# Kernel tuning notes

Measured on AMD Instinct MI355X. Metric: run time of the kernel, lower is better.

The kernel has to match this reference:

```python
import jax, jax.numpy as jnp
import numpy as np

NBINS = 256

def _equalize_flat(flat):
    # flat: [N, P] int32 pixel values in [0,255], N = B*C channels, P = H*W pixels
    N, P = flat.shape
    hist = jax.vmap(lambda v: jnp.bincount(v, length=NBINS))(flat)  # [N, 256]
    bins = jnp.arange(NBINS, dtype=jnp.int32)
    # last nonzero bin value per channel (PIL: drop last nonzero entry from the step sum)
    last_idx = jnp.max(jnp.where(hist != 0, bins[None, :], -1), axis=1)  # [N]
    last_val = jnp.take_along_axis(hist, last_idx[:, None], axis=1)[:, 0]  # [N]
    step = (P - last_val) // 255  # [N] integer floor div
    safe_step = jnp.maximum(step, 1)
    cs = jnp.cumsum(hist, axis=1)  # [N, 256]
    lut = (cs + (step // 2)[:, None]) // safe_step[:, None]
    # pad left with 0, drop last, clamp to [0,255]
    lut = jnp.concatenate([jnp.zeros((N, 1), lut.dtype), lut[:, :-1]], axis=1)
    lut = jnp.clip(lut, 0, 255)
    eq = jnp.take_along_axis(lut, flat, axis=1)  # [N, P]
    # channels with step==0 pass through unchanged
    return jnp.where((step == 0)[:, None], flat, eq)


def setup_inputs() -> dict:
    key = jax.random.key(0)
    img = jax.random.randint(key, (64, 3, 512, 512), 0, 256).astype(jnp.float32)
    return {"img": img}


def reference(img) -> jnp.ndarray:
    B, C, H, W = img.shape
    flat = img.astype(jnp.int32).reshape(B * C, H * W)
    out = _equalize_flat(flat)
    return out.reshape(B, C, H, W).astype(img.dtype)
```

## Files before the change

### kernel.cpp

```cpp
#include <hip/hip_runtime.h>


#define NBINS 256
#define BPC 32

__global__ __launch_bounds__(256) void eq_hist_kernel(
    const float* __restrict__ in, unsigned int* __restrict__ ghist,
    int P, int bpc) {
    __shared__ unsigned int lh[NBINS * 32];
    const int t = threadIdx.x;
    const int copy = t & 31;

    for (int i = t; i < NBINS * 32; i += 256) lh[i] = 0u;
    __syncthreads();

    const int chan = blockIdx.x / bpc;
    const int blk  = blockIdx.x % bpc;
    const int chunk = P / bpc;
    const float4* base =
        (const float4*)(in + (size_t)chan * P + (size_t)blk * chunk);
    const int nvec = chunk / 4;

    for (int i = t; i < nvec; i += 256) {
        float4 v = base[i];
        int ix = min(max((int)v.x, 0), 255);
        int iy = min(max((int)v.y, 0), 255);
        int iz = min(max((int)v.z, 0), 255);
        int iw = min(max((int)v.w, 0), 255);
        atomicAdd(&lh[ix * 32 + copy], 1u);
        atomicAdd(&lh[iy * 32 + copy], 1u);
        atomicAdd(&lh[iz * 32 + copy], 1u);
        atomicAdd(&lh[iw * 32 + copy], 1u);
    }
    __syncthreads();

    unsigned int s = 0;
    #pragma unroll
    for (int c = 0; c < 32; ++c)
        s += lh[t * 32 + ((t + c) & 31)];
    atomicAdd(&ghist[chan * NBINS + t], s);
}

__global__ __launch_bounds__(256) void eq_lut_kernel(
    const unsigned int* __restrict__ ghist, float* __restrict__ glut, int P) {
    __shared__ unsigned int s[NBINS];
    __shared__ int sidx[NBINS];
    const int t = threadIdx.x;
    const int chan = blockIdx.x;

    unsigned int h = ghist[chan * NBINS + t];
    s[t] = h;
    sidx[t] = (h != 0u) ? t : -1;
    __syncthreads();

    for (int off = 128; off > 0; off >>= 1) {
        if (t < off) sidx[t] = max(sidx[t], sidx[t + off]);
        __syncthreads();
    }
    const int last_idx = sidx[0];
    const unsigned int last_val = s[last_idx];
    const int step = (P - (int)last_val) / 255;

    for (int off = 1; off < NBINS; off <<= 1) {
        unsigned int val = (t >= off) ? s[t - off] : 0u;
        __syncthreads();
        s[t] += val;
        __syncthreads();
    }

    float lv;
    if (step == 0) {
        lv = (float)t;
    } else {
        int cs_prev = (t == 0) ? 0 : (int)s[t - 1];
        int l = (cs_prev + (step >> 1)) / step;
        l = min(max(l, 0), 255);
        lv = (float)l;
    }
    glut[chan * NBINS + t] = lv;
}

__global__ __launch_bounds__(256) void eq_apply_kernel(
    const float* __restrict__ in, const float* __restrict__ glut,
    float* __restrict__ out, int P, int bpc) {
    __shared__ float slut[NBINS];
    const int t = threadIdx.x;
    const int chan = blockIdx.x / bpc;
    const int blk  = blockIdx.x % bpc;

    slut[t] = glut[chan * NBINS + t];
    __syncthreads();

    const int chunk = P / bpc;
    const size_t base = (size_t)chan * P + (size_t)blk * chunk;
    const float4* vin = (const float4*)(in + base);
    float4* vout = (float4*)(out + base);
    const int nvec = chunk / 4;

    for (int i = t; i < nvec; i += 256) {
        float4 v = vin[i];
        float4 r;
        r.x = slut[min(max((int)v.x, 0), 255)];
        r.y = slut[min(max((int)v.y, 0), 255)];
        r.z = slut[min(max((int)v.z, 0), 255)];
        r.w = slut[min(max((int)v.w, 0), 255)];
        vout[i] = r;
    }
}

extern "C" void kernel_launch(void* const* d_in, const int* in_sizes, int n_in,
                              void* d_out, int out_size, void* d_ws, size_t ws_size,
                              hipStream_t stream) {
    const float* img = (const float*)d_in[0];
    float* out = (float*)d_out;

    const int P = 512 * 512;
    const int total = in_sizes[0];
    const int N = total / P;

    unsigned int* ghist = (unsigned int*)d_ws;
    float* glut = (float*)((char*)d_ws + (size_t)N * NBINS * sizeof(unsigned int));

    hipMemsetAsync(d_ws, 0, (size_t)N * NBINS * sizeof(unsigned int), stream);

    eq_hist_kernel<<<N * BPC, 256, 0, stream>>>(img, ghist, P, BPC);
    eq_lut_kernel<<<N, 256, 0, stream>>>(ghist, glut, P);
    eq_apply_kernel<<<N * BPC, 256, 0, stream>>>(img, glut, out, P, BPC);
}
```

Before: 371.6 us.

## Pack pixel bytes during histogram pass and apply LUT from packed buffer

The histogram kernel now also writes each pixel as a byte into a packed uint32 workspace buffer. The apply kernel reads this quarter-size buffer instead of re-reading the float image. Per-block partial histograms are written without global atomics and summed in the LUT kernel, which removes the memset. This cuts global read traffic in the apply pass, at the cost of an extra write in the histogram pass and more workspace memory.

```diff
diff --git a/kernel.cpp b/kernel.cpp
--- a/kernel.cpp
+++ b/kernel.cpp
@@ -4,9 +4,9 @@
 #define NBINS 256
 #define BPC 32
 
-__global__ __launch_bounds__(256) void eq_hist_kernel(
-    const float* __restrict__ in, unsigned int* __restrict__ ghist,
-    int P, int bpc) {
+__global__ __launch_bounds__(256) void eq_hist_pack_kernel(
+    const float* __restrict__ in, unsigned int* __restrict__ phist,
+    unsigned int* __restrict__ packed, int P, int bpc) {
     __shared__ unsigned int lh[NBINS * 32];
     const int t = threadIdx.x;
     const int copy = t & 31;
@@ -17,20 +17,22 @@
     const int chan = blockIdx.x / bpc;
     const int blk  = blockIdx.x % bpc;
     const int chunk = P / bpc;
-    const float4* base =
-        (const float4*)(in + (size_t)chan * P + (size_t)blk * chunk);
+    const size_t base = (size_t)chan * P + (size_t)blk * chunk;
+    const float4* vin = (const float4*)(in + base);
+    unsigned int* pout = packed + base / 4;
     const int nvec = chunk / 4;
 
     for (int i = t; i < nvec; i += 256) {
-        float4 v = base[i];
-        int ix = min(max((int)v.x, 0), 255);
-        int iy = min(max((int)v.y, 0), 255);
-        int iz = min(max((int)v.z, 0), 255);
-        int iw = min(max((int)v.w, 0), 255);
+        float4 v = vin[i];
+        unsigned int ix = (unsigned int)min(max((int)v.x, 0), 255);
+        unsigned int iy = (unsigned int)min(max((int)v.y, 0), 255);
+        unsigned int iz = (unsigned int)min(max((int)v.z, 0), 255);
+        unsigned int iw = (unsigned int)min(max((int)v.w, 0), 255);
         atomicAdd(&lh[ix * 32 + copy], 1u);
         atomicAdd(&lh[iy * 32 + copy], 1u);
         atomicAdd(&lh[iz * 32 + copy], 1u);
         atomicAdd(&lh[iw * 32 + copy], 1u);
+        pout[i] = ix | (iy << 8) | (iz << 16) | (iw << 24);
     }
     __syncthreads();
 
@@ -38,17 +40,20 @@
     #pragma unroll
     for (int c = 0; c < 32; ++c)
         s += lh[t * 32 + ((t + c) & 31)];
-    atomicAdd(&ghist[chan * NBINS + t], s);
+    phist[(size_t)blockIdx.x * NBINS + t] = s;
 }
 
 __global__ __launch_bounds__(256) void eq_lut_kernel(
-    const unsigned int* __restrict__ ghist, float* __restrict__ glut, int P) {
+    const unsigned int* __restrict__ phist, float* __restrict__ glut,
+    int P, int bpc) {
     __shared__ unsigned int s[NBINS];
     __shared__ int sidx[NBINS];
     const int t = threadIdx.x;
     const int chan = blockIdx.x;
 
-    unsigned int h = ghist[chan * NBINS + t];
+    unsigned int h = 0;
+    const unsigned int* pbase = phist + (size_t)chan * bpc * NBINS;
+    for (int b = 0; b < bpc; ++b) h += pbase[b * NBINS + t];
     s[t] = h;
     sidx[t] = (h != 0u) ? t : -1;
     __syncthreads();
@@ -81,7 +86,7 @@
 }
 
 __global__ __launch_bounds__(256) void eq_apply_kernel(
-    const float* __restrict__ in, const float* __restrict__ glut,
+    const unsigned int* __restrict__ packed, const float* __restrict__ glut,
     float* __restrict__ out, int P, int bpc) {
     __shared__ float slut[NBINS];
     const int t = threadIdx.x;
@@ -93,18 +98,25 @@
 
     const int chunk = P / bpc;
     const size_t base = (size_t)chan * P + (size_t)blk * chunk;
-    const float4* vin = (const float4*)(in + base);
+    const uint4* pin = (const uint4*)(packed + base / 4);
     float4* vout = (float4*)(out + base);
-    const int nvec = chunk / 4;
+    const int nq = chunk / 16;
 
-    for (int i = t; i < nvec; i += 256) {
-        float4 v = vin[i];
-        float4 r;
-        r.x = slut[min(max((int)v.x, 0), 255)];
-        r.y = slut[min(max((int)v.y, 0), 255)];
-        r.z = slut[min(max((int)v.z, 0), 255)];
-        r.w = slut[min(max((int)v.w, 0), 255)];
-        vout[i] = r;
+    for (int i = t; i < nq; i += 256) {
+        uint4 p = pin[i];
+        float4 r0, r1, r2, r3;
+        r0.x = slut[p.x & 255u];  r0.y = slut[(p.x >> 8) & 255u];
+        r0.z = slut[(p.x >> 16) & 255u];  r0.w = slut[p.x >> 24];
+        r1.x = slut[p.y & 255u];  r1.y = slut[(p.y >> 8) & 255u];
+        r1.z = slut[(p.y >> 16) & 255u];  r1.w = slut[p.y >> 24];
+        r2.x = slut[p.z & 255u];  r2.y = slut[(p.z >> 8) & 255u];
+        r2.z = slut[(p.z >> 16) & 255u];  r2.w = slut[p.z >> 24];
+        r3.x = slut[p.w & 255u];  r3.y = slut[(p.w >> 8) & 255u];
+        r3.z = slut[(p.w >> 16) & 255u];  r3.w = slut[p.w >> 24];
+        vout[i * 4 + 0] = r0;
+        vout[i * 4 + 1] = r1;
+        vout[i * 4 + 2] = r2;
+        vout[i * 4 + 3] = r3;
     }
 }
 
@@ -118,12 +130,12 @@
     const int total = in_sizes[0];
     const int N = total / P;
 
-    unsigned int* ghist = (unsigned int*)d_ws;
-    float* glut = (float*)((char*)d_ws + (size_t)N * NBINS * sizeof(unsigned int));
+    unsigned int* packed = (unsigned int*)d_ws;
+    unsigned int* phist  = (unsigned int*)((char*)d_ws + (size_t)total);
+    float* glut = (float*)((char*)phist +
+                           (size_t)N * BPC * NBINS * sizeof(unsigned int));
 
-    hipMemsetAsync(d_ws, 0, (size_t)N * NBINS * sizeof(unsigned int), stream);
-
-    eq_hist_kernel<<<N * BPC, 256, 0, stream>>>(img, ghist, P, BPC);
-    eq_lut_kernel<<<N, 256, 0, stream>>>(ghist, glut, P);
-    eq_apply_kernel<<<N * BPC, 256, 0, stream>>>(img, glut, out, P, BPC);
+    eq_hist_pack_kernel<<<N * BPC, 256, 0, stream>>>(img, phist, packed, P, BPC);
+    eq_lut_kernel<<<N, 256, 0, stream>>>(phist, glut, P, BPC);
+    eq_apply_kernel<<<N * BPC, 256, 0, stream>>>(packed, glut, out, P, BPC);
 }
```

New measurement: 384.4 us. +3.4%, slower.

## Replace global atomics with per-block partial histograms, replicate LUT, nontemporal stores

Applied to the files above, without the earlier changes.

Histogram blocks now write per-block partial histograms, which the LUT kernel sums. This removes the memset and the global atomics. The apply kernel replicates the LUT 32 times in shared memory to cut bank conflicts on gathers, and writes the output with nontemporal stores to avoid polluting the cache. In exchange it needs more workspace, the LUT kernel does 32 reads per bin, and the apply kernel uses more shared memory, which could lower occupancy.

```diff
diff --git a/kernel.cpp b/kernel.cpp
--- a/kernel.cpp
+++ b/kernel.cpp
@@ -4,8 +4,10 @@
 #define NBINS 256
 #define BPC 32
 
+typedef float vfloat4 __attribute__((ext_vector_type(4)));
+
 __global__ __launch_bounds__(256) void eq_hist_kernel(
-    const float* __restrict__ in, unsigned int* __restrict__ ghist,
+    const float* __restrict__ in, unsigned int* __restrict__ phist,
     int P, int bpc) {
     __shared__ unsigned int lh[NBINS * 32];
     const int t = threadIdx.x;
@@ -17,12 +19,12 @@
     const int chan = blockIdx.x / bpc;
     const int blk  = blockIdx.x % bpc;
     const int chunk = P / bpc;
-    const float4* base =
-        (const float4*)(in + (size_t)chan * P + (size_t)blk * chunk);
+    const size_t base = (size_t)chan * P + (size_t)blk * chunk;
+    const float4* vin = (const float4*)(in + base);
     const int nvec = chunk / 4;
 
     for (int i = t; i < nvec; i += 256) {
-        float4 v = base[i];
+        float4 v = vin[i];
         int ix = min(max((int)v.x, 0), 255);
         int iy = min(max((int)v.y, 0), 255);
         int iz = min(max((int)v.z, 0), 255);
@@ -38,17 +40,20 @@
     #pragma unroll
     for (int c = 0; c < 32; ++c)
         s += lh[t * 32 + ((t + c) & 31)];
-    atomicAdd(&ghist[chan * NBINS + t], s);
+    phist[(size_t)blockIdx.x * NBINS + t] = s;
 }
 
 __global__ __launch_bounds__(256) void eq_lut_kernel(
-    const unsigned int* __restrict__ ghist, float* __restrict__ glut, int P) {
+    const unsigned int* __restrict__ phist, float* __restrict__ glut,
+    int P, int bpc) {
     __shared__ unsigned int s[NBINS];
     __shared__ int sidx[NBINS];
     const int t = threadIdx.x;
     const int chan = blockIdx.x;
 
-    unsigned int h = ghist[chan * NBINS + t];
+    unsigned int h = 0;
+    const unsigned int* pbase = phist + (size_t)chan * bpc * NBINS;
+    for (int b = 0; b < bpc; ++b) h += pbase[b * NBINS + t];
     s[t] = h;
     sidx[t] = (h != 0u) ? t : -1;
     __syncthreads();
@@ -83,28 +88,32 @@
 __global__ __launch_bounds__(256) void eq_apply_kernel(
     const float* __restrict__ in, const float* __restrict__ glut,
     float* __restrict__ out, int P, int bpc) {
-    __shared__ float slut[NBINS];
+    __shared__ float slut[NBINS * 32];
     const int t = threadIdx.x;
+    const int copy = t & 31;
     const int chan = blockIdx.x / bpc;
     const int blk  = blockIdx.x % bpc;
 
-    slut[t] = glut[chan * NBINS + t];
+    const float lv = glut[chan * NBINS + t];
+    #pragma unroll
+    for (int c = 0; c < 32; ++c)
+        slut[t * 32 + ((t + c) & 31)] = lv;
     __syncthreads();
 
     const int chunk = P / bpc;
     const size_t base = (size_t)chan * P + (size_t)blk * chunk;
     const float4* vin = (const float4*)(in + base);
-    float4* vout = (float4*)(out + base);
+    vfloat4* vout = (vfloat4*)(out + base);
     const int nvec = chunk / 4;
 
     for (int i = t; i < nvec; i += 256) {
         float4 v = vin[i];
-        float4 r;
-        r.x = slut[min(max((int)v.x, 0), 255)];
-        r.y = slut[min(max((int)v.y, 0), 255)];
-        r.z = slut[min(max((int)v.z, 0), 255)];
-        r.w = slut[min(max((int)v.w, 0), 255)];
-        vout[i] = r;
+        vfloat4 r;
+        r.x = slut[min(max((int)v.x, 0), 255) * 32 + copy];
+        r.y = slut[min(max((int)v.y, 0), 255) * 32 + copy];
+        r.z = slut[min(max((int)v.z, 0), 255) * 32 + copy];
+        r.w = slut[min(max((int)v.w, 0), 255) * 32 + copy];
+        __builtin_nontemporal_store(r, &vout[i]);
     }
 }
 
@@ -118,12 +127,11 @@
     const int total = in_sizes[0];
     const int N = total / P;
 
-    unsigned int* ghist = (unsigned int*)d_ws;
-    float* glut = (float*)((char*)d_ws + (size_t)N * NBINS * sizeof(unsigned int));
+    unsigned int* phist = (unsigned int*)d_ws;
+    float* glut = (float*)((char*)d_ws +
+                           (size_t)N * BPC * NBINS * sizeof(unsigned int));
 
-    hipMemsetAsync(d_ws, 0, (size_t)N * NBINS * sizeof(unsigned int), stream);
-
-    eq_hist_kernel<<<N * BPC, 256, 0, stream>>>(img, ghist, P, BPC);
-    eq_lut_kernel<<<N, 256, 0, stream>>>(ghist, glut, P);
+    eq_hist_kernel<<<N * BPC, 256, 0, stream>>>(img, phist, P, BPC);
+    eq_lut_kernel<<<N, 256, 0, stream>>>(phist, glut, P, BPC);
     eq_apply_kernel<<<N * BPC, 256, 0, stream>>>(img, glut, out, P, BPC);
 }
```

After: 367.6 us. Within noise of the previous version (-1.1%).
